# Kernel tuning notes

Measured on AMD Instinct MI355X. Metric: run time of the kernel, lower is better.

Reference implementation:

```python
import jax, jax.numpy as jnp
import numpy as np

B, N = 2, 2048
DIM, NH, DH = 640, 10, 64
DINNER = 2560
L = 4
DEMB = 32
NTOKS = [128, 64]
NFEAT = 19
FDIM = 280
FEATD = DIM - DEMB * len(NTOKS)  # 576
SQRTD = float(np.sqrt(DH))


def _ln(x, g, b, eps=1e-5):
    m = jnp.mean(x, -1, keepdims=True)
    v = jnp.var(x, -1, keepdims=True)
    return (x - m) * jax.lax.rsqrt(v + eps) * g + b


def setup_inputs() -> dict:
    key = jax.random.key(0)
    ks = iter(jax.random.split(key, 32))
    s = 0.05
    return {
        "x_feats": jax.random.normal(next(ks), (B, N, NFEAT), jnp.float32),
        "x_toks": jax.random.randint(next(ks), (B, N, 2), 0, 64),
        "mask": jnp.ones((B, N), jnp.float32),
        "emb0": jax.random.normal(next(ks), (NTOKS[0] + 1, DEMB)) * s,
        "emb1": jax.random.normal(next(ks), (NTOKS[1] + 1, DEMB)) * s,
        "feat_w": jax.random.normal(next(ks), (FEATD, NFEAT)) * s,
        "feat_b": jnp.zeros((FEATD,)),
        "qkv_w": jax.random.normal(next(ks), (L, 3 * DIM, DIM)) * s,
        "qkv_b": jnp.zeros((L, 3 * DIM)),
        "o_w": jax.random.normal(next(ks), (L, DIM, DIM)) * s,
        "ln1_g": jnp.ones((L, DIM)), "ln1_b": jnp.zeros((L, DIM)),
        "ln2_g": jnp.ones((L, DIM)), "ln2_b": jnp.zeros((L, DIM)),
        "p1_w": jax.random.normal(next(ks), (L, DINNER, DIM)) * s,
        "p1_b": jnp.zeros((L, DINNER)),
        "p2_w": jax.random.normal(next(ks), (L, DIM, DINNER)) * s,
        "p2_b": jnp.zeros((L, DIM)),
        "fn_g": jnp.ones((DIM,)), "fn_b": jnp.zeros((DIM,)),
        "lin1_w": jax.random.normal(next(ks), (FDIM, DIM)) * s,
        "lin1_b": jnp.zeros((FDIM,)),
        "rb1_w": jax.random.normal(next(ks), (FDIM, FDIM)) * s,
        "rb1_b": jnp.zeros((FDIM,)),
        "rb2_w": jax.random.normal(next(ks), (FDIM, FDIM)) * s,
        "rb2_b": jnp.zeros((FDIM,)),
        "out_w": jax.random.normal(next(ks), (1, FDIM)) * s,
        "out_b": jnp.zeros((1,)),
    }


def _forward(x_feats, x_toks, mask, emb0, emb1, feat_w, feat_b,
             qkv_w, qkv_b, o_w, ln1_g, ln1_b, ln2_g, ln2_b,
             p1_w, p1_b, p2_w, p2_b, fn_g, fn_b,
             lin1_w, lin1_b, rb1_w, rb1_b, rb2_w, rb2_b, out_w, out_b):
    # mask outer product [B,N,N]; additive mask 0 where allowed, -1e20 elsewhere
    mask2 = jnp.einsum('bi,bj->bij', mask, mask)
    add_mask = jnp.where(mask2 > 0, 0.0, -1e20)

    # embeddings + feature projection -> [B,N,DIM]
    Z = jnp.concatenate([emb0[x_toks[..., 0]], emb1[x_toks[..., 1]],
                         x_feats @ feat_w.T + feat_b], axis=-1)

    def layer(Z, prm):
        qw, qb, ow, g1, b1, g2, b2, w1, c1, w2, c2 = prm
        inp = Z
        Zn = _ln(Z, g1, b1)
        # qkv reshaped to [B,N,H,3*DH], chunked along last dim: V, Q, K
        qkv = (Zn @ qw.T + qb).reshape(B, N, NH, 3 * DH)
        V, Q, K = qkv[..., :DH], qkv[..., DH:2 * DH], qkv[..., 2 * DH:]
        W = jnp.einsum('bnhd,bmhd->bhnm', Q, K) / SQRTD + add_mask[:, None]
        W = jax.nn.softmax(W, axis=3) * mask2[:, None]  # post-softmax mult mask
        attn = jnp.einsum('bhnm,bmhd->bnhd', W, V).reshape(B, N, DIM)
        Z = jax.nn.leaky_relu(attn) @ ow.T + inp  # leaky_relu BEFORE o_net
        inp = Z
        Zn = _ln(Z, g2, b2)
        Z = jax.nn.relu(Zn @ w1.T + c1) @ w2.T + c2 + inp
        return Z, None

    Z, _ = jax.lax.scan(layer, Z,
                        (qkv_w, qkv_b, o_w, ln1_g, ln1_b, ln2_g, ln2_b,
                         p1_w, p1_b, p2_w, p2_b))
    Z = _ln(Z, fn_g, fn_b)
    # ranking head: 1x1 convs == per-token linears
    h = Z @ lin1_w.T + lin1_b
    h = h + (jax.nn.relu(h @ rb1_w.T + rb1_b) @ rb2_w.T + rb2_b)
    return (h @ out_w.T + out_b)[..., 0]  # [B,N]


def reference(x_feats, x_toks, mask, emb0, emb1, feat_w, feat_b,
              qkv_w, qkv_b, o_w, ln1_g, ln1_b, ln2_g, ln2_b,
              p1_w, p1_b, p2_w, p2_b, fn_g, fn_b,
              lin1_w, lin1_b, rb1_w, rb1_b, rb2_w, rb2_b, out_w, out_b):
    return _forward(x_feats, x_toks, mask, emb0, emb1, feat_w, feat_b,
                    qkv_w, qkv_b, o_w, ln1_g, ln1_b, ln2_g, ln2_b,
                    p1_w, p1_b, p2_w, p2_b, fn_g, fn_b,
                    lin1_w, lin1_b, rb1_w, rb1_b, rb2_w, rb2_b, out_w, out_b)
```

## Files before the change

### kernel.cpp

```cpp
#include <hip/hip_runtime.h>

#define B_ 2
#define N_ 2048
#define DIM_ 640
#define NH_ 10
#define DH_ 64
#define DINNER_ 2560
#define L_ 4
#define FDIM_ 280
#define FDIMP_ 320
#define FEATD_ 576
#define NFEAT_ 19
#define ROWS_ (B_*N_)
#define NITS_ 16

typedef __attribute__((ext_vector_type(8))) unsigned short ushort8;
typedef __attribute__((ext_vector_type(4))) unsigned short ushort4v;
typedef __attribute__((ext_vector_type(8))) __bf16 bf16x8;
typedef __attribute__((ext_vector_type(4))) __bf16 bf16x4;
typedef __attribute__((ext_vector_type(4))) float f32x4;
typedef __attribute__((ext_vector_type(2))) unsigned int u32x2;

static __device__ __forceinline__ unsigned short f2bf(float f){
  unsigned int u = __builtin_bit_cast(unsigned int, f);
  u += 0x7fffu + ((u >> 16) & 1u);
  return (unsigned short)(u >> 16);
}

static __device__ __forceinline__ f32x4 mfma16(ushort8 a, ushort8 b, f32x4 c){
  return __builtin_amdgcn_mfma_f32_16x16x32_bf16(
      __builtin_bit_cast(bf16x8, a), __builtin_bit_cast(bf16x8, b), c, 0, 0, 0);
}

#define GLD(src,dst) __builtin_amdgcn_global_load_lds((const __attribute__((address_space(1))) void*)(src), (__attribute__((address_space(3))) void*)(dst), 16, 0, 0)

#define SEG0 4915200
#define SEG1 1638400
#define SEG2 6553600
#define SEG3 6553600
#define SEG4 179200
#define SEG5 89600
#define SEG6 89600
#define SEG7 655360
#define SEG8 655360
#define SEG9 4096
#define E0 SEG0
#define E1 (E0+SEG1)
#define E2 (E1+SEG2)
#define E3 (E2+SEG3)
#define E4 (E3+SEG4)
#define E5 (E4+SEG5)
#define E6 (E5+SEG6)
#define E7 (E6+SEG7)
#define E8 (E7+SEG8)
#define E9 (E8+SEG9)

__global__ __launch_bounds__(256) void prep_kernel(
    const float* __restrict__ qkv_w, const float* __restrict__ o_w,
    const float* __restrict__ p1_w, const float* __restrict__ p2_w,
    const float* __restrict__ lin1_w, const float* __restrict__ rb1_w,
    const float* __restrict__ rb2_w, const float* __restrict__ mask,
    unsigned short* __restrict__ qkvw, unsigned short* __restrict__ oww,
    unsigned short* __restrict__ p1w, unsigned short* __restrict__ p2w,
    unsigned short* __restrict__ l1w, unsigned short* __restrict__ r1w,
    unsigned short* __restrict__ r2w, unsigned int* __restrict__ hb1z,
    unsigned int* __restrict__ hb2z, float* __restrict__ mbb)
{
  for (int i = blockIdx.x*256 + threadIdx.x; i < E9; i += gridDim.x*256){
    int j = i;
    if (j < E0) { qkvw[j] = f2bf(qkv_w[j]); continue; }
    j -= E0;
    if (j < SEG1) { oww[j] = f2bf(o_w[j]); continue; }
    j -= SEG1;
    if (j < SEG2) { p1w[j] = f2bf(p1_w[j]); continue; }
    j -= SEG2;
    if (j < SEG3) { p2w[j] = f2bf(p2_w[j]); continue; }
    j -= SEG3;
    if (j < SEG4) { l1w[j] = f2bf(lin1_w[j]); continue; }
    j -= SEG4;
    if (j < SEG5) { int r = j/FDIMP_, c = j - r*FDIMP_;
                    r1w[j] = (c<FDIM_) ? f2bf(rb1_w[r*FDIM_+c]) : (unsigned short)0; continue; }
    j -= SEG5;
    if (j < SEG6) { int r = j/FDIMP_, c = j - r*FDIMP_;
                    r2w[j] = (c<FDIM_) ? f2bf(rb2_w[r*FDIM_+c]) : (unsigned short)0; continue; }
    j -= SEG6;
    if (j < SEG7) { hb1z[j] = 0u; continue; }
    j -= SEG7;
    if (j < SEG8) { hb2z[j] = 0u; continue; }
    j -= SEG8;
    mbb[j] = (mask[j] > 0.f) ? 0.f : -1e30f;
  }
}

__global__ __launch_bounds__(256) void embed_kernel(const float* __restrict__ xf,
    const int* __restrict__ xt, const float* __restrict__ e0, const float* __restrict__ e1,
    const float* __restrict__ fw, const float* __restrict__ fb, float* __restrict__ Z){
  int row = blockIdx.x;
  __shared__ float f[NFEAT_];
  int t = threadIdx.x;
  if (t < NFEAT_) f[t] = xf[row*NFEAT_ + t];
  __syncthreads();
  if (t < 32) {
    int tok0 = xt[row*2];
    Z[(size_t)row*DIM_ + t] = e0[tok0*32 + t];
  } else if (t < 64) {
    int tok1 = xt[row*2+1];
    Z[(size_t)row*DIM_ + t] = e1[tok1*32 + (t-32)];
  }
  for (int fo = t; fo < FEATD_; fo += 256){
    float acc = fb[fo];
    #pragma unroll
    for (int k=0;k<NFEAT_;k++) acc += f[k]*fw[fo*NFEAT_+k];
    Z[(size_t)row*DIM_ + 64 + fo] = acc;
  }
}

__global__ __launch_bounds__(256) void ln_kernel(const float* __restrict__ X,
    const float* __restrict__ g, const float* __restrict__ bb,
    unsigned short* __restrict__ out){
  int lane = threadIdx.x & 63;
  int row = blockIdx.x*4 + (threadIdx.x >> 6);
  const float* x = X + (size_t)row*DIM_;
  float v[10]; float s=0.f, sq=0.f;
  #pragma unroll
  for (int j=0;j<10;j++){ float t = x[lane + j*64]; v[j]=t; s+=t; sq+=t*t; }
  #pragma unroll
  for (int off=1; off<64; off<<=1){ s += __shfl_xor(s, off, 64); sq += __shfl_xor(sq, off, 64); }
  float mean = s*(1.f/DIM_);
  float var = sq*(1.f/DIM_) - mean*mean;
  float rstd = rsqrtf(var + 1e-5f);
  unsigned short* o = out + (size_t)row*DIM_;
  #pragma unroll
  for (int j=0;j<10;j++){ int c = lane + j*64; o[c] = f2bf((v[j]-mean)*rstd*g[c] + bb[c]); }
}

template<bool BIAS, bool RELU, bool RES, bool OUTF, bool OUTB>
__global__ __launch_bounds__(256) void gemm_kernel(
    const unsigned short* __restrict__ A, int lda,
    const unsigned short* __restrict__ Bw, int ldb,
    const float* __restrict__ bias,
    const float* __restrict__ Res, int ldres,
    float* __restrict__ Cf, int ldcf,
    unsigned short* __restrict__ Cb, int ldcb,
    int Ncols, int K)
{
  __shared__ __align__(16) unsigned short As[3][128*32];
  __shared__ __align__(16) unsigned short Bs[3][128*32];
  int t = threadIdx.x;
  int wid = t >> 6, lane = t & 63;
  int wr = wid >> 1, wc = wid & 1;
  int lg = lane >> 4, lm = lane & 15;
  int row0 = blockIdx.y * 128;
  int col0 = blockIdx.x * 128;

  int c0 = wid*128 + lane, c1 = c0 + 64;
  int ar0 = c0 >> 2, aq0 = c0 & 3;
  int ar1 = c1 >> 2, aq1 = c1 & 3;
  const unsigned short* a0 = A + (size_t)(row0+ar0)*lda + aq0*8;
  const unsigned short* a1 = A + (size_t)(row0+ar1)*lda + aq1*8;
  int br0 = col0+ar0; if (br0 >= Ncols) br0 = Ncols-1;
  int br1 = col0+ar1; if (br1 >= Ncols) br1 = Ncols-1;
  const unsigned short* b0 = Bw + (size_t)br0*ldb + aq0*8;
  const unsigned short* b1 = Bw + (size_t)br1*ldb + aq1*8;

  f32x4 acc[4][4];
  #pragma unroll
  for (int m=0;m<4;m++)
    #pragma unroll
    for (int n=0;n<4;n++) acc[m][n] = f32x4{0.f,0.f,0.f,0.f};

  int nk = K >> 5;
  GLD(a0, &As[0][c0*8]); GLD(b0, &Bs[0][c0*8]);
  GLD(a1, &As[0][c1*8]); GLD(b1, &Bs[0][c1*8]);
  if (nk > 1){
    GLD(a0+32, &As[1][c0*8]); GLD(b0+32, &Bs[1][c0*8]);
    GLD(a1+32, &As[1][c1*8]); GLD(b1+32, &Bs[1][c1*8]);
  }

  int cur = 0;
  for (int tk=0; tk<nk; ++tk){
    if (tk+2 < nk){
      int st = (cur >= 1) ? cur-1 : 2;
      int koff = (tk+2) << 5;
      GLD(a0+koff, &As[st][c0*8]); GLD(b0+koff, &Bs[st][c0*8]);
      GLD(a1+koff, &As[st][c1*8]); GLD(b1+koff, &Bs[st][c1*8]);
    }
    int rem = nk-1-tk;
    if (rem > 1)       asm volatile("s_waitcnt vmcnt(8)" ::: "memory");
    else if (rem == 1) asm volatile("s_waitcnt vmcnt(4)" ::: "memory");
    else               asm volatile("s_waitcnt vmcnt(0)" ::: "memory");
    __builtin_amdgcn_s_barrier();
    asm volatile("" ::: "memory");
    const unsigned short* Ac = &As[cur][0];
    const unsigned short* Bc = &Bs[cur][0];
    ushort8 af[4], bfr[4];
    #pragma unroll
    for (int m=0;m<4;m++) af[m] = *(const ushort8*)(Ac + (wr*64 + m*16 + lm)*32 + lg*8);
    #pragma unroll
    for (int n=0;n<4;n++) bfr[n] = *(const ushort8*)(Bc + (wc*64 + n*16 + lm)*32 + lg*8);
    #pragma unroll
    for (int m=0;m<4;m++)
      #pragma unroll
      for (int n=0;n<4;n++)
        acc[m][n] = mfma16(af[m], bfr[n], acc[m][n]);
    asm volatile("" ::: "memory");
    __builtin_amdgcn_s_barrier();
    cur = (cur == 2) ? 0 : cur+1;
  }

  #pragma unroll
  for (int m=0;m<4;m++){
    int rbase = row0 + wr*64 + m*16 + lg*4;
    #pragma unroll
    for (int n=0;n<4;n++){
      int cc = col0 + wc*64 + n*16 + lm;
      if (cc < Ncols){
        float bv = 0.f;
        if (BIAS) bv = bias[cc];
        #pragma unroll
        for (int rr=0;rr<4;rr++){
          float v = acc[m][n][rr] + bv;
          if (RELU) v = fmaxf(v, 0.f);
          if (RES) v += Res[(size_t)(rbase+rr)*ldres + cc];
          if (OUTF) Cf[(size_t)(rbase+rr)*ldcf + cc] = v;
          if (OUTB) Cb[(size_t)(rbase+rr)*ldcb + cc] = f2bf(v);
        }
      }
    }
  }
}

template<bool BIAS, bool RELU, bool RES, bool OUTF, bool OUTB>
__global__ __launch_bounds__(256) void gemm64_kernel(
    const unsigned short* __restrict__ A, int lda,
    const unsigned short* __restrict__ Bw, int ldb,
    const float* __restrict__ bias,
    const float* __restrict__ Res, int ldres,
    float* __restrict__ Cf, int ldcf,
    unsigned short* __restrict__ Cb, int ldcb,
    int Ncols, int K)
{
  __shared__ __align__(16) unsigned short As[3][64*64];
  __shared__ __align__(16) unsigned short Bs[3][64*64];
  int t = threadIdx.x;
  int wid = t >> 6, lane = t & 63;
  int wr = wid >> 1, wc = wid & 1;
  int lg = lane >> 4, lm = lane & 15;
  int row0 = blockIdx.y * 64;
  int col0 = blockIdx.x * 64;

  int ar0 = t >> 3, aq = t & 7;
  int ar1 = ar0 + 32;
  const unsigned short* a0 = A + (size_t)(row0+ar0)*lda + aq*8;
  const unsigned short* a1 = A + (size_t)(row0+ar1)*lda + aq*8;
  int br0 = col0+ar0; if (br0 >= Ncols) br0 = Ncols-1;
  int br1 = col0+ar1; if (br1 >= Ncols) br1 = Ncols-1;
  const unsigned short* b0 = Bw + (size_t)br0*ldb + aq*8;
  const unsigned short* b1 = Bw + (size_t)br1*ldb + aq*8;
  int l0 = ar0*64 + aq*8, l1 = ar1*64 + aq*8;

  f32x4 acc[2][2];
  #pragma unroll
  for (int m=0;m<2;m++)
    #pragma unroll
    for (int n=0;n<2;n++) acc[m][n] = f32x4{0.f,0.f,0.f,0.f};

  int nk = K >> 6;
  GLD(a0, &As[0][l0]); GLD(b0, &Bs[0][l0]);
  GLD(a1, &As[0][l1]); GLD(b1, &Bs[0][l1]);
  if (nk > 1){
    GLD(a0+64, &As[1][l0]); GLD(b0+64, &Bs[1][l0]);
    GLD(a1+64, &As[1][l1]); GLD(b1+64, &Bs[1][l1]);
  }

  int cur = 0;
  for (int tk=0; tk<nk; ++tk){
    if (tk+2 < nk){
      int st = (cur >= 1) ? cur-1 : 2;
      int koff = (tk+2) << 6;
      GLD(a0+koff, &As[st][l0]); GLD(b0+koff, &Bs[st][l0]);
      GLD(a1+koff, &As[st][l1]); GLD(b1+koff, &Bs[st][l1]);
    }
    int rem = nk-1-tk;
    if (rem > 1)       asm volatile("s_waitcnt vmcnt(8)" ::: "memory");
    else if (rem == 1) asm volatile("s_waitcnt vmcnt(4)" ::: "memory");
    else               asm volatile("s_waitcnt vmcnt(0)" ::: "memory");
    __builtin_amdgcn_s_barrier();
    asm volatile("" ::: "memory");
    const unsigned short* Ac = &As[cur][0];
    const unsigned short* Bc = &Bs[cur][0];
    ushort8 af[2][2], bfr[2][2];
    #pragma unroll
    for (int kk=0;kk<2;kk++){
      #pragma unroll
      for (int m=0;m<2;m++) af[kk][m] = *(const ushort8*)(Ac + (wr*32 + m*16 + lm)*64 + kk*32 + lg*8);
      #pragma unroll
      for (int n=0;n<2;n++) bfr[kk][n] = *(const ushort8*)(Bc + (wc*32 + n*16 + lm)*64 + kk*32 + lg*8);
    }
    #pragma unroll
    for (int kk=0;kk<2;kk++)
      #pragma unroll
      for (int m=0;m<2;m++)
        #pragma unroll
        for (int n=0;n<2;n++)
          acc[m][n] = mfma16(af[kk][m], bfr[kk][n], acc[m][n]);
    asm volatile("" ::: "memory");
    __builtin_amdgcn_s_barrier();
    cur = (cur == 2) ? 0 : cur+1;
  }

  #pragma unroll
  for (int m=0;m<2;m++){
    int rbase = row0 + wr*32 + m*16 + lg*4;
    #pragma unroll
    for (int n=0;n<2;n++){
      int cc = col0 + wc*32 + n*16 + lm;
      if (cc < Ncols){
        float bv = 0.f;
        if (BIAS) bv = bias[cc];
        #pragma unroll
        for (int rr=0;rr<4;rr++){
          float v = acc[m][n][rr] + bv;
          if (RELU) v = fmaxf(v, 0.f);
          if (RES) v += Res[(size_t)(rbase+rr)*ldres + cc];
          if (OUTF) Cf[(size_t)(rbase+rr)*ldcf + cc] = v;
          if (OUTB) Cb[(size_t)(rbase+rr)*ldcb + cc] = f2bf(v);
        }
      }
    }
  }
}

__global__ __launch_bounds__(256) void attn_kernel(const unsigned short* __restrict__ qkv,
    const float* __restrict__ mb, float* __restrict__ op, float* __restrict__ lpp){
  int bh = blockIdx.y; int b = bh/NH_, h = bh%NH_;
  int t = threadIdx.x; int wid = t>>6, lane = t&63, lg = lane>>4, lm = lane&15;
  int q0 = blockIdx.x*64 + wid*16;
  int it0 = blockIdx.z * NITS_;
  size_t prow = (size_t)blockIdx.z*ROWS_ + b*N_;

  __shared__ __align__(128) unsigned short Ks[2][4096];
  __shared__ __align__(128) unsigned short Vs[2][4096];
  __shared__ __align__(16) float maskL[NITS_*64];

  const size_t base = (size_t)b*N_*1920 + (size_t)h*192;
  const size_t kvoff = (size_t)it0*64*1920;

  int c0 = t, c1 = t+256;
  int kk0 = c0>>3, kc0 = (c0&7)^(kk0&7);
  int kk1 = c1>>3, kc1 = (c1&7)^(kk1&7);
  const unsigned short* kS0 = qkv + base + kvoff + 128 + (size_t)kk0*1920 + kc0*8;
  const unsigned short* kS1 = qkv + base + kvoff + 128 + (size_t)kk1*1920 + kc1*8;
  int vk0 = ((c0>>5)<<2)|((c0>>1)&3), vd0 = (((c0>>3)&3)<<1)|(c0&1);
  int vk1 = ((c1>>5)<<2)|((c1>>1)&3), vd1 = (((c1>>3)&3)<<1)|(c1&1);
  const unsigned short* vS0 = qkv + base + kvoff + (size_t)vk0*1920 + vd0*8;
  const unsigned short* vS1 = qkv + base + kvoff + (size_t)vk1*1920 + vd1*8;

  ushort8 qf[2];
  #pragma unroll
  for (int ss=0; ss<2; ss++)
    qf[ss] = *(const ushort8*)(qkv + base + (size_t)(q0+lm)*1920 + 64 + ss*32 + lg*8);
  float cb2 = mb[b*N_ + q0 + lm] - 17.3123405f;

  GLD(mb + b*N_ + it0*64 + t*4, &maskL[t*4]);
  GLD(kS0, &Ks[0][c0*8]); GLD(kS1, &Ks[0][c1*8]);
  GLD(vS0, &Vs[0][c0*8]); GLD(vS1, &Vs[0][c1*8]);

  float lp = 0.f;
  f32x4 o[4];
  #pragma unroll
  for (int dn=0;dn<4;dn++) o[dn] = f32x4{0.f,0.f,0.f,0.f};

  for (int ii=0; ii<NITS_; ++ii){
    int cur = ii & 1;
    if (ii < NITS_ - 1){
      const size_t adv = (size_t)(ii+1)*64*1920;
      GLD(kS0+adv, &Ks[1-cur][c0*8]); GLD(kS1+adv, &Ks[1-cur][c1*8]);
      GLD(vS0+adv, &Vs[1-cur][c0*8]); GLD(vS1+adv, &Vs[1-cur][c1*8]);
      asm volatile("s_waitcnt vmcnt(4)" ::: "memory");
    } else {
      asm volatile("s_waitcnt vmcnt(0)" ::: "memory");
    }
    __builtin_amdgcn_s_barrier();
    asm volatile("" ::: "memory");

    const unsigned short* Kc = &Ks[cur][0];
    f32x4 sf[4];
    #pragma unroll
    for (int c=0;c<4;c++){
      int krow = c*16 + lm;
      f32x4 s = f32x4{0.f,0.f,0.f,0.f};
      #pragma unroll
      for (int ss=0;ss<2;ss++){
        ushort8 kf = *(const ushort8*)(Kc + (krow*8 + ((ss*4+lg)^(krow&7)))*8);
        s = mfma16(kf, qf[ss], s);
      }
      sf[c] = s;
    }
    f32x4 mkv[4];
    #pragma unroll
    for (int c=0;c<4;c++) mkv[c] = *(const f32x4*)&maskL[ii*64 + c*16 + lg*4];

    unsigned vsb = (unsigned)(size_t)(__attribute__((address_space(3))) unsigned short*)&Vs[cur][0];
    unsigned a0 = vsb + lg*512 + lm*8;
    u32x2 vb[4][4];
    asm volatile(
      "ds_read_b64_tr_b16 %0, %4 offset:0\n\t"
      "ds_read_b64_tr_b16 %1, %4 offset:128\n\t"
      "ds_read_b64_tr_b16 %2, %4 offset:256\n\t"
      "ds_read_b64_tr_b16 %3, %4 offset:384"
      : "=&v"(vb[0][0]),"=&v"(vb[0][1]),"=&v"(vb[0][2]),"=&v"(vb[0][3]) : "v"(a0));
    asm volatile(
      "ds_read_b64_tr_b16 %0, %4 offset:2048\n\t"
      "ds_read_b64_tr_b16 %1, %4 offset:2176\n\t"
      "ds_read_b64_tr_b16 %2, %4 offset:2304\n\t"
      "ds_read_b64_tr_b16 %3, %4 offset:2432"
      : "=&v"(vb[1][0]),"=&v"(vb[1][1]),"=&v"(vb[1][2]),"=&v"(vb[1][3]) : "v"(a0));
    asm volatile(
      "ds_read_b64_tr_b16 %0, %4 offset:4096\n\t"
      "ds_read_b64_tr_b16 %1, %4 offset:4224\n\t"
      "ds_read_b64_tr_b16 %2, %4 offset:4352\n\t"
      "ds_read_b64_tr_b16 %3, %4 offset:4480"
      : "=&v"(vb[2][0]),"=&v"(vb[2][1]),"=&v"(vb[2][2]),"=&v"(vb[2][3]) : "v"(a0));
    asm volatile(
      "ds_read_b64_tr_b16 %0, %4 offset:6144\n\t"
      "ds_read_b64_tr_b16 %1, %4 offset:6272\n\t"
      "ds_read_b64_tr_b16 %2, %4 offset:6400\n\t"
      "ds_read_b64_tr_b16 %3, %4 offset:6528"
      : "=&v"(vb[3][0]),"=&v"(vb[3][1]),"=&v"(vb[3][2]),"=&v"(vb[3][3]) : "v"(a0));

    float pm[4][4]; bf16x4 pa[4];
    #pragma unroll
    for (int c=0;c<4;c++){
      #pragma unroll
      for (int r=0;r<4;r++){
        float x = fmaf(sf[c][r], 0.18033688f, cb2 + mkv[c][r]);
        pm[c][r] = __builtin_amdgcn_exp2f(x);
      }
      lp += (pm[c][0]+pm[c][1]) + (pm[c][2]+pm[c][3]);
      pa[c] = bf16x4{(__bf16)pm[c][0], (__bf16)pm[c][1], (__bf16)pm[c][2], (__bf16)pm[c][3]};
    }

#define PVM(dn_, c_) asm("v_mfma_f32_16x16x16_bf16 %0, %1, %2, %0" \
      : "+v"(o[dn_]) : "v"(__builtin_bit_cast(u32x2, pa[c_])), "v"(vb[c_][dn_]))
    asm volatile("s_waitcnt lgkmcnt(8)" ::: "memory");
    __builtin_amdgcn_sched_barrier(0);
    __builtin_amdgcn_s_setprio(1);
    PVM(0,0); PVM(1,0); PVM(2,0); PVM(3,0);
    PVM(0,1); PVM(1,1); PVM(2,1); PVM(3,1);
    asm volatile("s_waitcnt lgkmcnt(0)" ::: "memory");
    __builtin_amdgcn_sched_barrier(0);
    PVM(0,2); PVM(1,2); PVM(2,2); PVM(3,2);
    PVM(0,3); PVM(1,3); PVM(2,3); PVM(3,3);
    __builtin_amdgcn_s_setprio(0);
#undef PVM
    asm volatile("" ::: "memory");
    __builtin_amdgcn_s_barrier();
  }

  float s = lp;
  s += __shfl_xor(s, 16, 64);
  s += __shfl_xor(s, 32, 64);
  if (lg == 0) lpp[(prow + q0 + lm)*NH_ + h] = s;
  #pragma unroll
  for (int r=0;r<4;r++){
    float* ob = op + (prow + q0 + lg*4 + r)*DIM_ + h*64;
    #pragma unroll
    for (int dn=0;dn<4;dn++)
      ob[dn*16 + lm] = o[dn][r];
  }
}

__global__ __launch_bounds__(256) void attnred_kernel(const float* __restrict__ op,
    const float* __restrict__ lpp, unsigned short* __restrict__ att){
  int idx = blockIdx.x*256 + threadIdx.x;
  int row = idx / 160;
  int c4 = (idx - row*160) * 4;
  int h = c4 >> 6;
  f32x4 o0 = *(const f32x4*)(op + (size_t)row*DIM_ + c4);
  f32x4 o1 = *(const f32x4*)(op + ((size_t)ROWS_ + row)*DIM_ + c4);
  float l = lpp[row*NH_ + h] + lpp[(ROWS_ + row)*NH_ + h];
  float inv = 1.0f / fmaxf(l, 1e-30f);
  ushort4v rr;
  #pragma unroll
  for (int j=0;j<4;j++){
    float v = (o0[j] + o1[j]) * inv;
    v = (v >= 0.f) ? v : 0.01f*v;
    rr[j] = f2bf(v);
  }
  *(ushort4v*)(att + (size_t)row*DIM_ + c4) = rr;
}

__global__ __launch_bounds__(256) void out_kernel(const float* __restrict__ hf,
    const float* __restrict__ ow, const float* __restrict__ ob, float* __restrict__ out){
  int lane = threadIdx.x & 63;
  int row = blockIdx.x*4 + (threadIdx.x>>6);
  const float* x = hf + (size_t)row*FDIM_;
  float s = 0.f;
  for (int j=lane;j<FDIM_;j+=64) s += x[j]*ow[j];
  #pragma unroll
  for (int off=1; off<64; off<<=1) s += __shfl_xor(s, off, 64);
  if (lane==0) out[row] = s + ob[0];
}

extern "C" void kernel_launch(void* const* d_in, const int* in_sizes, int n_in,
                              void* d_out, int out_size, void* d_ws, size_t ws_size,
                              hipStream_t stream)
{
  const float* x_feats = (const float*)d_in[0];
  const int*   x_toks  = (const int*)d_in[1];
  const float* mask    = (const float*)d_in[2];
  const float* emb0    = (const float*)d_in[3];
  const float* emb1    = (const float*)d_in[4];
  const float* feat_w  = (const float*)d_in[5];
  const float* feat_b  = (const float*)d_in[6];
  const float* qkv_w   = (const float*)d_in[7];
  const float* qkv_b   = (const float*)d_in[8];
  const float* o_w     = (const float*)d_in[9];
  const float* ln1_g   = (const float*)d_in[10];
  const float* ln1_b   = (const float*)d_in[11];
  const float* ln2_g   = (const float*)d_in[12];
  const float* ln2_b   = (const float*)d_in[13];
  const float* p1_w    = (const float*)d_in[14];
  const float* p1_b    = (const float*)d_in[15];
  const float* p2_w    = (const float*)d_in[16];
  const float* p2_b    = (const float*)d_in[17];
  const float* fn_g    = (const float*)d_in[18];
  const float* fn_b    = (const float*)d_in[19];
  const float* lin1_w  = (const float*)d_in[20];
  const float* lin1_b  = (const float*)d_in[21];
  const float* rb1_w   = (const float*)d_in[22];
  const float* rb1_b   = (const float*)d_in[23];
  const float* rb2_w   = (const float*)d_in[24];
  const float* rb2_b   = (const float*)d_in[25];
  const float* out_w   = (const float*)d_in[26];
  const float* out_b   = (const float*)d_in[27];
  float* out = (float*)d_out;

  char* w = (char*)d_ws;
  auto alloc = [&](size_t bytes)->void*{ void* p = (void*)w; w += (bytes + 255) & ~(size_t)255; return p; };

  float* Z              = (float*)alloc((size_t)ROWS_*DIM_*4);
  unsigned short* Zn    = (unsigned short*)alloc((size_t)ROWS_*DIM_*2);
  unsigned short* qkvB  = (unsigned short*)alloc((size_t)ROWS_*1920*2);
  unsigned short* attB  = (unsigned short*)alloc((size_t)ROWS_*DIM_*2);
  unsigned short* Hb    = (unsigned short*)alloc((size_t)ROWS_*DINNER_*2);
  float* hf             = (float*)alloc((size_t)ROWS_*FDIM_*4);
  unsigned short* hb1   = (unsigned short*)alloc((size_t)ROWS_*FDIMP_*2);
  unsigned short* hb2   = (unsigned short*)alloc((size_t)ROWS_*FDIMP_*2);
  float* mbb            = (float*)alloc((size_t)ROWS_*4);
  float* opart          = (float*)alloc((size_t)2*ROWS_*DIM_*4);
  float* lpart          = (float*)alloc((size_t)2*ROWS_*NH_*4);
  unsigned short* qkvw  = (unsigned short*)alloc((size_t)L_*1920*DIM_*2);
  unsigned short* oww   = (unsigned short*)alloc((size_t)L_*DIM_*DIM_*2);
  unsigned short* p1w   = (unsigned short*)alloc((size_t)L_*DINNER_*DIM_*2);
  unsigned short* p2w   = (unsigned short*)alloc((size_t)L_*DIM_*DINNER_*2);
  unsigned short* l1w   = (unsigned short*)alloc((size_t)FDIM_*DIM_*2);
  unsigned short* r1w   = (unsigned short*)alloc((size_t)FDIM_*FDIMP_*2);
  unsigned short* r2w   = (unsigned short*)alloc((size_t)FDIM_*FDIMP_*2);

  prep_kernel<<<2048,256,0,stream>>>(qkv_w, o_w, p1_w, p2_w, lin1_w, rb1_w, rb2_w, mask,
      qkvw, oww, p1w, p2w, l1w, r1w, r2w,
      (unsigned int*)hb1, (unsigned int*)hb2, mbb);

  embed_kernel<<<ROWS_,256,0,stream>>>(x_feats, x_toks, emb0, emb1, feat_w, feat_b, Z);

  for (int l=0; l<L_; l++){
    ln_kernel<<<ROWS_/4,256,0,stream>>>(Z, ln1_g + l*DIM_, ln1_b + l*DIM_, Zn);
    gemm_kernel<true,false,false,false,true><<<dim3(15,32),256,0,stream>>>(
        Zn, DIM_, qkvw + (size_t)l*1920*DIM_, DIM_, qkv_b + l*1920,
        nullptr, 0, nullptr, 0, qkvB, 1920, 1920, DIM_);
    attn_kernel<<<dim3(N_/64, B_*NH_, 2),256,0,stream>>>(qkvB, mbb, opart, lpart);
    attnred_kernel<<<ROWS_*160/256,256,0,stream>>>(opart, lpart, attB);
    gemm64_kernel<false,false,true,true,false><<<dim3(10,64),256,0,stream>>>(
        attB, DIM_, oww + (size_t)l*DIM_*DIM_, DIM_, nullptr,
        Z, DIM_, Z, DIM_, nullptr, 0, DIM_, DIM_);
    ln_kernel<<<ROWS_/4,256,0,stream>>>(Z, ln2_g + l*DIM_, ln2_b + l*DIM_, Zn);
    gemm_kernel<true,true,false,false,true><<<dim3(20,32),256,0,stream>>>(
        Zn, DIM_, p1w + (size_t)l*DINNER_*DIM_, DIM_, p1_b + l*DINNER_,
        nullptr, 0, nullptr, 0, Hb, DINNER_, DINNER_, DIM_);
    gemm64_kernel<true,false,true,true,false><<<dim3(10,64),256,0,stream>>>(
        Hb, DINNER_, p2w + (size_t)l*DIM_*DINNER_, DINNER_, p2_b + l*DIM_,
        Z, DIM_, Z, DIM_, nullptr, 0, DIM_, DINNER_);
  }

  ln_kernel<<<ROWS_/4,256,0,stream>>>(Z, fn_g, fn_b, Zn);
  gemm64_kernel<true,false,false,true,true><<<dim3(5,64),256,0,stream>>>(
      Zn, DIM_, l1w, DIM_, lin1_b, nullptr, 0, hf, FDIM_, hb1, FDIMP_, FDIM_, DIM_);
  gemm64_kernel<true,true,false,false,true><<<dim3(5,64),256,0,stream>>>(
      hb1, FDIMP_, r1w, FDIMP_, rb1_b, nullptr, 0, nullptr, 0, hb2, FDIMP_, FDIM_, FDIMP_);
  gemm64_kernel<true,false,true,true,false><<<dim3(5,64),256,0,stream>>>(
      hb2, FDIMP_, r2w, FDIMP_, rb2_b, hf, FDIM_, hf, FDIM_, nullptr, 0, FDIM_, FDIMP_);
  out_kernel<<<ROWS_/4,256,0,stream>>>(hf, out_w, out_b, out);
}
```

Baseline: 715.1 us.

## Swizzle GEMM LDS tiles, double-buffer with K=64 steps in GEMM kernels

Both GEMM kernels switch from a triple-buffered LDS pipeline to double buffering. The 128x128 kernel's K step grows from 32 to 64, and LDS chunks are XOR-swizzled so the MFMA fragment reads avoid bank conflicts. This cuts LDS read conflicts and loop overhead per K step. The cost is a shallower prefetch depth, which may expose more global-load latency. The prep kernel's segment offset macros are also collapsed.

Result: faster. 678.5 us (-5.1%).

```diff
diff --git a/kernel.cpp b/kernel.cpp
--- a/kernel.cpp
+++ b/kernel.cpp
@@ -45,15 +45,7 @@
 #define SEG8 655360
 #define SEG9 4096
 #define E0 SEG0
-#define E1 (E0+SEG1)
-#define E2 (E1+SEG2)
-#define E3 (E2+SEG3)
-#define E4 (E3+SEG4)
-#define E5 (E4+SEG5)
-#define E6 (E5+SEG6)
-#define E7 (E6+SEG7)
-#define E8 (E7+SEG8)
-#define E9 (E8+SEG9)
+#define E9 (SEG0+SEG1+SEG2+SEG3+SEG4+SEG5+SEG6+SEG7+SEG8+SEG9)
 
 __global__ __launch_bounds__(256) void prep_kernel(
     const float* __restrict__ qkv_w, const float* __restrict__ o_w,
@@ -144,8 +136,8 @@
     unsigned short* __restrict__ Cb, int ldcb,
     int Ncols, int K)
 {
-  __shared__ __align__(16) unsigned short As[3][128*32];
-  __shared__ __align__(16) unsigned short Bs[3][128*32];
+  __shared__ __align__(128) unsigned short As[2][8192];
+  __shared__ __align__(128) unsigned short Bs[2][8192];
   int t = threadIdx.x;
   int wid = t >> 6, lane = t & 63;
   int wr = wid >> 1, wc = wid & 1;
@@ -153,15 +145,17 @@
   int row0 = blockIdx.y * 128;
   int col0 = blockIdx.x * 128;
 
-  int c0 = wid*128 + lane, c1 = c0 + 64;
-  int ar0 = c0 >> 2, aq0 = c0 & 3;
-  int ar1 = c1 >> 2, aq1 = c1 & 3;
-  const unsigned short* a0 = A + (size_t)(row0+ar0)*lda + aq0*8;
-  const unsigned short* a1 = A + (size_t)(row0+ar1)*lda + aq1*8;
-  int br0 = col0+ar0; if (br0 >= Ncols) br0 = Ncols-1;
-  int br1 = col0+ar1; if (br1 >= Ncols) br1 = Ncols-1;
-  const unsigned short* b0 = Bw + (size_t)br0*ldb + aq0*8;
-  const unsigned short* b1 = Bw + (size_t)br1*ldb + aq1*8;
+  const unsigned short* aSrc[4];
+  const unsigned short* bSrc[4];
+  #pragma unroll
+  for (int j=0;j<4;j++){
+    int s = t + j*256;
+    int r = s >> 3;
+    int c = (s & 7) ^ (((r >> 2) & 1) << 1);
+    aSrc[j] = A + (size_t)(row0 + r)*lda + c*8;
+    int br = col0 + r; if (br >= Ncols) br = Ncols - 1;
+    bSrc[j] = Bw + (size_t)br*ldb + c*8;
+  }
 
   f32x4 acc[4][4];
   #pragma unroll
@@ -169,43 +163,47 @@
     #pragma unroll
     for (int n=0;n<4;n++) acc[m][n] = f32x4{0.f,0.f,0.f,0.f};
 
-  int nk = K >> 5;
-  GLD(a0, &As[0][c0*8]); GLD(b0, &Bs[0][c0*8]);
-  GLD(a1, &As[0][c1*8]); GLD(b1, &Bs[0][c1*8]);
-  if (nk > 1){
-    GLD(a0+32, &As[1][c0*8]); GLD(b0+32, &Bs[1][c0*8]);
-    GLD(a1+32, &As[1][c1*8]); GLD(b1+32, &Bs[1][c1*8]);
-  }
-
-  int cur = 0;
+  int nk = K >> 6;
+  #pragma unroll
+  for (int j=0;j<4;j++){
+    GLD(aSrc[j], &As[0][(t + j*256)*8]);
+    GLD(bSrc[j], &Bs[0][(t + j*256)*8]);
+  }
+
+  int swz = (lm & 4) >> 1;
   for (int tk=0; tk<nk; ++tk){
-    if (tk+2 < nk){
-      int st = (cur >= 1) ? cur-1 : 2;
-      int koff = (tk+2) << 5;
-      GLD(a0+koff, &As[st][c0*8]); GLD(b0+koff, &Bs[st][c0*8]);
-      GLD(a1+koff, &As[st][c1*8]); GLD(b1+koff, &Bs[st][c1*8]);
-    }
-    int rem = nk-1-tk;
-    if (rem > 1)       asm volatile("s_waitcnt vmcnt(8)" ::: "memory");
-    else if (rem == 1) asm volatile("s_waitcnt vmcnt(4)" ::: "memory");
-    else               asm volatile("s_waitcnt vmcnt(0)" ::: "memory");
+    int cur = tk & 1;
+    if (tk+1 < nk){
+      int kt = (tk+1) << 6;
+      #pragma unroll
+      for (int j=0;j<4;j++){
+        GLD(aSrc[j]+kt, &As[cur^1][(t + j*256)*8]);
+        GLD(bSrc[j]+kt, &Bs[cur^1][(t + j*256)*8]);
+      }
+      asm volatile("s_waitcnt vmcnt(8)" ::: "memory");
+    } else {
+      asm volatile("s_waitcnt vmcnt(0)" ::: "memory");
+    }
     __builtin_amdgcn_s_barrier();
     asm volatile("" ::: "memory");
     const unsigned short* Ac = &As[cur][0];
     const unsigned short* Bc = &Bs[cur][0];
-    ushort8 af[4], bfr[4];
-    #pragma unroll
-    for (int m=0;m<4;m++) af[m] = *(const ushort8*)(Ac + (wr*64 + m*16 + lm)*32 + lg*8);
-    #pragma unroll
-    for (int n=0;n<4;n++) bfr[n] = *(const ushort8*)(Bc + (wc*64 + n*16 + lm)*32 + lg*8);
-    #pragma unroll
-    for (int m=0;m<4;m++)
-      #pragma unroll
-      for (int n=0;n<4;n++)
-        acc[m][n] = mfma16(af[m], bfr[n], acc[m][n]);
+    #pragma unroll
+    for (int kk=0;kk<2;kk++){
+      int ch = ((kk*4 + lg) ^ swz) * 8;
+      ushort8 af[4], bfr[4];
+      #pragma unroll
+      for (int m=0;m<4;m++) af[m] = *(const ushort8*)(Ac + (wr*64 + m*16 + lm)*64 + ch);
+      #pragma unroll
+      for (int n=0;n<4;n++) bfr[n] = *(const ushort8*)(Bc + (wc*64 + n*16 + lm)*64 + ch);
+      #pragma unroll
+      for (int m=0;m<4;m++)
+        #pragma unroll
+        for (int n=0;n<4;n++)
+          acc[m][n] = mfma16(af[m], bfr[n], acc[m][n]);
+    }
     asm volatile("" ::: "memory");
     __builtin_amdgcn_s_barrier();
-    cur = (cur == 2) ? 0 : cur+1;
   }
 
   #pragma unroll
@@ -240,8 +238,8 @@
     unsigned short* __restrict__ Cb, int ldcb,
     int Ncols, int K)
 {
-  __shared__ __align__(16) unsigned short As[3][64*64];
-  __shared__ __align__(16) unsigned short Bs[3][64*64];
+  __shared__ __align__(128) unsigned short As[2][64*64];
+  __shared__ __align__(128) unsigned short Bs[2][64*64];
   int t = threadIdx.x;
   int wid = t >> 6, lane = t & 63;
   int wr = wid >> 1, wc = wid & 1;
@@ -249,15 +247,16 @@
   int row0 = blockIdx.y * 64;
   int col0 = blockIdx.x * 64;
 
-  int ar0 = t >> 3, aq = t & 7;
+  int ar0 = t >> 3;
   int ar1 = ar0 + 32;
+  int aq = (t & 7) ^ (((ar0 >> 2) & 1) << 1);
   const unsigned short* a0 = A + (size_t)(row0+ar0)*lda + aq*8;
   const unsigned short* a1 = A + (size_t)(row0+ar1)*lda + aq*8;
   int br0 = col0+ar0; if (br0 >= Ncols) br0 = Ncols-1;
   int br1 = col0+ar1; if (br1 >= Ncols) br1 = Ncols-1;
   const unsigned short* b0 = Bw + (size_t)br0*ldb + aq*8;
   const unsigned short* b1 = Bw + (size_t)br1*ldb + aq*8;
-  int l0 = ar0*64 + aq*8, l1 = ar1*64 + aq*8;
+  int l0 = t*8, l1 = (t+256)*8;
 
   f32x4 acc[2][2];
   #pragma unroll
@@ -268,45 +267,38 @@
   int nk = K >> 6;
   GLD(a0, &As[0][l0]); GLD(b0, &Bs[0][l0]);
   GLD(a1, &As[0][l1]); GLD(b1, &Bs[0][l1]);
-  if (nk > 1){
-    GLD(a0+64, &As[1][l0]); GLD(b0+64, &Bs[1][l0]);
-    GLD(a1+64, &As[1][l1]); GLD(b1+64, &Bs[1][l1]);
-  }
-
-  int cur = 0;
+
+  int swz = (lm & 4) >> 1;
   for (int tk=0; tk<nk; ++tk){
-    if (tk+2 < nk){
-      int st = (cur >= 1) ? cur-1 : 2;
-      int koff = (tk+2) << 6;
-      GLD(a0+koff, &As[st][l0]); GLD(b0+koff, &Bs[st][l0]);
-      GLD(a1+koff, &As[st][l1]); GLD(b1+koff, &Bs[st][l1]);
-    }
-    int rem = nk-1-tk;
-    if (rem > 1)       asm volatile("s_waitcnt vmcnt(8)" ::: "memory");
-    else if (rem == 1) asm volatile("s_waitcnt vmcnt(4)" ::: "memory");
-    else               asm volatile("s_waitcnt vmcnt(0)" ::: "memory");
+    int cur = tk & 1;
+    if (tk+1 < nk){
+      int koff = (tk+1) << 6;
+      GLD(a0+koff, &As[cur^1][l0]); GLD(b0+koff, &Bs[cur^1][l0]);
+      GLD(a1+koff, &As[cur^1][l1]); GLD(b1+koff, &Bs[cur^1][l1]);
+      asm volatile("s_waitcnt vmcnt(4)" ::: "memory");
+    } else {
+      asm volatile("s_waitcnt vmcnt(0)" ::: "memory");
+    }
     __builtin_amdgcn_s_barrier();
     asm volatile("" ::: "memory");
     const unsigned short* Ac = &As[cur][0];
     const unsigned short* Bc = &Bs[cur][0];
-    ushort8 af[2][2], bfr[2][2];
     #pragma unroll
     for (int kk=0;kk<2;kk++){
-      #pragma unroll
-      for (int m=0;m<2;m++) af[kk][m] = *(const ushort8*)(Ac + (wr*32 + m*16 + lm)*64 + kk*32 + lg*8);
-      #pragma unroll
-      for (int n=0;n<2;n++) bfr[kk][n] = *(const ushort8*)(Bc + (wc*32 + n*16 + lm)*64 + kk*32 + lg*8);
-    }
-    #pragma unroll
-    for (int kk=0;kk<2;kk++)
+      int ch = ((kk*4 + lg) ^ swz) * 8;
+      ushort8 af[2], bfr[2];
+      #pragma unroll
+      for (int m=0;m<2;m++) af[m] = *(const ushort8*)(Ac + (wr*32 + m*16 + lm)*64 + ch);
+      #pragma unroll
+      for (int n=0;n<2;n++) bfr[n] = *(const ushort8*)(Bc + (wc*32 + n*16 + lm)*64 + ch);
       #pragma unroll
       for (int m=0;m<2;m++)
         #pragma unroll
         for (int n=0;n<2;n++)
-          acc[m][n] = mfma16(af[kk][m], bfr[kk][n], acc[m][n]);
+          acc[m][n] = mfma16(af[m], bfr[n], acc[m][n]);
+    }
     asm volatile("" ::: "memory");
     __builtin_amdgcn_s_barrier();
-    cur = (cur == 2) ? 0 : cur+1;
   }
 
   #pragma unroll
```
